# Optimization experiments

Measured on AMD Instinct MI355X. Metric: run time of the kernel, lower is better.

## Reference

```python
import jax, jax.numpy as jnp
import numpy as np

M, N, D, P = 16, 4096, 128, 8192
H = N // D


def setup_inputs() -> dict:
    key = jax.random.key(0)
    ks = jax.random.split(key, 6)
    return {
        "X": jax.random.normal(ks[0], (M, N), dtype=jnp.float32),
        "W_q": jax.random.normal(ks[1], (N, N), dtype=jnp.float32) / np.sqrt(N),
        "W_k": jax.random.normal(ks[2], (N, N), dtype=jnp.float32) / np.sqrt(N),
        "W_v": jax.random.normal(ks[3], (N, N), dtype=jnp.float32) / np.sqrt(N),
        "cache_K": jax.random.normal(ks[4], (H, P, D), dtype=jnp.float32),
        "cache_V": jax.random.normal(ks[5], (H, P, D), dtype=jnp.float32),
    }


def _rms(x):
    # unaffine RMS norm over last dim, no eps (matches torch source)
    return x * jax.lax.rsqrt(jnp.mean(jnp.square(x), axis=-1, keepdims=True))


def reference(X, W_q, W_k, W_v, cache_K, cache_V):
    m, n = X.shape
    h, p, d = cache_K.shape
    # QKV projections -> [H, M, D]
    q = (X @ W_q).reshape(m, h, d).swapaxes(0, 1)
    k = (X @ W_k).reshape(m, h, d).swapaxes(0, 1)
    v = (X @ W_v).reshape(m, h, d).swapaxes(0, 1)
    q_norm = _rms(q)
    k_norm = _rms(k)
    # prepend KV cache: [H, P+M, D]
    k_cache = jnp.concatenate([cache_K[:, :p, :], k_norm], axis=1)
    v_cache = jnp.concatenate([cache_V[:, :p, :], v], axis=1)
    # attention WITHOUT 1/sqrt(D) scaling (matches torch source)
    scores = jnp.einsum("hmd,hpd->hmp", q_norm, k_cache)
    weights = jax.nn.softmax(scores, axis=-1)
    out = jnp.einsum("hmp,hpd->hmd", weights, v_cache)  # [H, M, D]
    return out.swapaxes(0, 1).reshape(m, n)
```

## Files before the change

### kernel.cpp

```cpp
#include <hip/hip_runtime.h>
#include <hip/hip_bf16.h>
#include <math.h>

#define M_ 16
#define N_ 4096
#define D_ 128
#define P_ 8192
#define H_ 32

#define NIC 32
#define ICH (N_/NIC)
#define NCB 16

#define CHUNK 64
#define NCH (P_/CHUNK)
#define NCH1 (NCH+1)

#define QKV_SZ       (3*H_*M_*D_)
#define PART_OFF     (QKV_SZ)
#define OPART_OFF    (QKV_SZ)
#define OPART_HALFSZ ((H_*NCH1*M_*D_)/2)
#define ML_OFF       (OPART_OFF + OPART_HALFSZ)

__global__ __launch_bounds__(256) void k_proj(const float* __restrict__ X,
                                              const float* __restrict__ Wq,
                                              const float* __restrict__ Wk,
                                              const float* __restrict__ Wv,
                                              float* __restrict__ part) {
  const int mat = blockIdx.z;
  const float* __restrict__ W = (mat == 0) ? Wq : ((mat == 1) ? Wk : Wv);
  const int cb = blockIdx.x, ic = blockIdx.y;
  const int t = threadIdx.x;
  const int j0 = cb * 256 + t;
  const int i0 = ic * ICH;

  __shared__ __align__(16) float XT[ICH][20];

  {
    const int i_l = t & 127, mh = t >> 7;
#pragma unroll
    for (int r = 0; r < 8; ++r)
      XT[i_l][mh * 8 + r] = X[(size_t)(mh * 8 + r) * N_ + i0 + i_l];
  }
  __syncthreads();

  float acc[16];
#pragma unroll
  for (int m = 0; m < 16; ++m) acc[m] = 0.f;

#pragma unroll 8
  for (int i = 0; i < ICH; ++i) {
    const float wv = __builtin_nontemporal_load(W + (size_t)(i0 + i) * N_ + j0);
    float xr[16];
    {
      float4 xv;
      xv = *reinterpret_cast<const float4*>(&XT[i][0]);
      xr[0] = xv.x; xr[1] = xv.y; xr[2] = xv.z; xr[3] = xv.w;
      xv = *reinterpret_cast<const float4*>(&XT[i][4]);
      xr[4] = xv.x; xr[5] = xv.y; xr[6] = xv.z; xr[7] = xv.w;
      xv = *reinterpret_cast<const float4*>(&XT[i][8]);
      xr[8] = xv.x; xr[9] = xv.y; xr[10] = xv.z; xr[11] = xv.w;
      xv = *reinterpret_cast<const float4*>(&XT[i][12]);
      xr[12] = xv.x; xr[13] = xv.y; xr[14] = xv.z; xr[15] = xv.w;
    }
#pragma unroll
    for (int m = 0; m < 16; ++m) acc[m] = fmaf(xr[m], wv, acc[m]);
  }

#pragma unroll
  for (int m = 0; m < 16; ++m)
    __builtin_nontemporal_store(acc[m], part + (size_t)((mat * NIC + ic) * M_ + m) * N_ + j0);
}

__global__ __launch_bounds__(256) void k_reduce(const float* __restrict__ part,
                                                float* __restrict__ qkv) {
  const int mat = blockIdx.z, m = blockIdx.y, nc = blockIdx.x;
  const int t = threadIdx.x;
  const int n = nc * 256 + t;

  float s = 0.f;
#pragma unroll
  for (int ic = 0; ic < NIC; ++ic)
    s += __builtin_nontemporal_load(part + (size_t)((mat * NIC + ic) * M_ + m) * N_ + n);

  float ss = s * s;
#pragma unroll
  for (int off = 1; off < 64; off <<= 1) ss += __shfl_xor(ss, off);
  __shared__ float wsum[4];
  const int wave = t >> 6, lane = t & 63;
  if (lane == 0) wsum[wave] = ss;
  __syncthreads();
  const int half = t >> 7;
  const float tot = wsum[half * 2] + wsum[half * 2 + 1];
  const float scale = (mat < 2) ? rsqrtf(tot * (1.0f / 128.0f)) : 1.0f;

  const int h = n >> 7, d = n & 127;
  qkv[(size_t)((mat * H_ + h) * M_ + m) * D_ + d] = s * scale;
}

__device__ __forceinline__ float fold8(float a[8], int dq) {
#pragma unroll
  for (int i = 0; i < 4; ++i) {
    const float send = (dq & 4) ? a[i] : a[i + 4];
    const float recv = __shfl_xor(send, 4);
    a[i] = ((dq & 4) ? a[i + 4] : a[i]) + recv;
  }
#pragma unroll
  for (int i = 0; i < 2; ++i) {
    const float send = (dq & 2) ? a[i] : a[i + 2];
    const float recv = __shfl_xor(send, 2);
    a[i] = ((dq & 2) ? a[i + 2] : a[i]) + recv;
  }
  {
    const float send = (dq & 1) ? a[0] : a[1];
    const float recv = __shfl_xor(send, 1);
    a[0] = ((dq & 1) ? a[1] : a[0]) + recv;
  }
  return a[0];
}

__device__ __forceinline__ unsigned pk2(float a, float b) {
  __hip_bfloat16 ha = __float2bfloat16(a), hb = __float2bfloat16(b);
  const unsigned short ua = *reinterpret_cast<unsigned short*>(&ha);
  const unsigned short ub = *reinterpret_cast<unsigned short*>(&hb);
  return (unsigned)ua | ((unsigned)ub << 16);
}

__global__ __attribute__((amdgpu_waves_per_eu(2, 8)))
__launch_bounds__(256) void k_attn(const float* __restrict__ cacheK,
                                   const float* __restrict__ cacheV,
                                   const float* __restrict__ qkv,
                                   __hip_bfloat16* __restrict__ opart,
                                   float* __restrict__ ml) {
  const int c = blockIdx.x, h = blockIdx.y;
  const int t = threadIdx.x;
  const int wave = t >> 6, lane = t & 63;
  const int valid = (c < NCH) ? CHUNK : M_;
  const float* __restrict__ Ksrc = (c < NCH)
      ? (cacheK + ((size_t)h * P_ + (size_t)c * CHUNK) * D_)
      : (qkv + (size_t)((1 * H_ + h) * M_) * D_);
  const float* __restrict__ Vsrc = (c < NCH)
      ? (cacheV + ((size_t)h * P_ + (size_t)c * CHUNK) * D_)
      : (qkv + (size_t)((2 * H_ + h) * M_) * D_);

  __shared__ __align__(16) float smem[4096];
  __shared__ __align__(16) float wx[4 * 128];
  __shared__ __align__(16) float mlx[4][8][2];

  float* qs = smem;
  float* wxp = wx + wave * 128;

  {
    const float4* src = reinterpret_cast<const float4*>(qkv + (size_t)(h * M_) * D_);
    reinterpret_cast<float4*>(qs)[t] = src[t];
    reinterpret_cast<float4*>(qs)[t + 256] = src[t + 256];
  }
  __syncthreads();

  const int pg = lane >> 3, dq = lane & 7;
  const int dl = lane * 2;
  const int rg = wave >> 1, mbase = (wave & 1) * 8;
  const int rbase = rg * 32;
  int rc = valid - rbase; rc = (rc < 0) ? 0 : ((rc > 32) ? 32 : rc);
  const int nb = rc >> 3;

  float mrun = -3.0e38f, lrun = 0.f;
  float2 o[8];
#pragma unroll
  for (int mi = 0; mi < 8; ++mi) o[mi] = make_float2(0.f, 0.f);

#pragma unroll 1
  for (int b = 0; b < nb; ++b) {
    const int r0 = rbase + b * 8;

    float4 kk0, kk1, kk2, kk3;
    {
      const float* ka = Ksrc + (size_t)(r0 + pg) * D_ + dq * 4;
      kk0 = *reinterpret_cast<const float4*>(ka);
      kk1 = *reinterpret_cast<const float4*>(ka + 32);
      kk2 = *reinterpret_cast<const float4*>(ka + 64);
      kk3 = *reinterpret_cast<const float4*>(ka + 96);
    }
    float2 vv[8];
#pragma unroll
    for (int j = 0; j < 8; ++j)
      vv[j] = *reinterpret_cast<const float2*>(Vsrc + (size_t)(r0 + j) * D_ + dl);

    float a[8];
#pragma unroll
    for (int mi = 0; mi < 8; ++mi) {
      const float* qrow = qs + (mbase + mi) * D_ + dq * 4;
      const float4 q0 = *reinterpret_cast<const float4*>(qrow);
      const float4 q1 = *reinterpret_cast<const float4*>(qrow + 32);
      const float4 q2 = *reinterpret_cast<const float4*>(qrow + 64);
      const float4 q3 = *reinterpret_cast<const float4*>(qrow + 96);
      float s;
      s = q0.x * kk0.x;
      s = fmaf(q0.y, kk0.y, s); s = fmaf(q0.z, kk0.z, s); s = fmaf(q0.w, kk0.w, s);
      s = fmaf(q1.x, kk1.x, s); s = fmaf(q1.y, kk1.y, s);
      s = fmaf(q1.z, kk1.z, s); s = fmaf(q1.w, kk1.w, s);
      s = fmaf(q2.x, kk2.x, s); s = fmaf(q2.y, kk2.y, s);
      s = fmaf(q2.z, kk2.z, s); s = fmaf(q2.w, kk2.w, s);
      s = fmaf(q3.x, kk3.x, s); s = fmaf(q3.y, kk3.y, s);
      s = fmaf(q3.z, kk3.z, s); s = fmaf(q3.w, kk3.w, s);
      a[mi] = s;
    }

    const float sA = fold8(a, dq);
    float tmax = sA;
    tmax = fmaxf(tmax, __shfl_xor(tmax, 8));
    tmax = fmaxf(tmax, __shfl_xor(tmax, 16));
    tmax = fmaxf(tmax, __shfl_xor(tmax, 32));
    const float mnew = fmaxf(mrun, tmax);
    const float fc = __expf(mrun - mnew);
    mrun = mnew;
    const float wA = __expf(sA - mnew);
    float rs = wA;
    rs += __shfl_xor(rs, 8); rs += __shfl_xor(rs, 16); rs += __shfl_xor(rs, 32);
    lrun = lrun * fc + rs;

    wxp[pg * 8 + dq] = wA;

#pragma unroll
    for (int mi = 0; mi < 8; ++mi) {
      const float fcm = __shfl(fc, (lane & 56) | mi);
      o[mi].x *= fcm; o[mi].y *= fcm;
    }

#pragma unroll
    for (int j = 0; j < 8; ++j) {
      const float4 w0 = *reinterpret_cast<const float4*>(&wxp[j * 8]);
      const float4 w1 = *reinterpret_cast<const float4*>(&wxp[j * 8 + 4]);
      const float2 v = vv[j];
#define PVM(i, wc) o[i].x = fmaf(wc, v.x, o[i].x); o[i].y = fmaf(wc, v.y, o[i].y);
      PVM(0, w0.x) PVM(1, w0.y) PVM(2, w0.z) PVM(3, w0.w)
      PVM(4, w1.x) PVM(5, w1.y) PVM(6, w1.z) PVM(7, w1.w)
#undef PVM
    }
  }

  __syncthreads();
  float* obuf = smem;
#pragma unroll
  for (int mi = 0; mi < 8; ++mi)
    *reinterpret_cast<float2*>(&obuf[wave * 1024 + mi * 128 + dl]) = o[mi];
  if (lane < 8) { mlx[wave][lane][0] = mrun; mlx[wave][lane][1] = lrun; }
  __syncthreads();

  {
    const int mm = t >> 4, seg = t & 15;
    const int mh = mm >> 3, mi = mm & 7;
    const float m0v = mlx[mh][mi][0], m1v = mlx[2 + mh][mi][0];
    const float mstar = fmaxf(m0v, m1v);
    const float e0 = __expf(m0v - mstar), e1 = __expf(m1v - mstar);
    const float T = mlx[mh][mi][1] * e0 + mlx[2 + mh][mi][1] * e1;
    const float4 a0 = *reinterpret_cast<const float4*>(&obuf[mh * 1024 + mi * 128 + seg * 8]);
    const float4 a1 = *reinterpret_cast<const float4*>(&obuf[mh * 1024 + mi * 128 + seg * 8 + 4]);
    const float4 b0 = *reinterpret_cast<const float4*>(&obuf[(2 + mh) * 1024 + mi * 128 + seg * 8]);
    const float4 b1 = *reinterpret_cast<const float4*>(&obuf[(2 + mh) * 1024 + mi * 128 + seg * 8 + 4]);
    float r0 = e0 * a0.x + e1 * b0.x, r1 = e0 * a0.y + e1 * b0.y;
    float r2 = e0 * a0.z + e1 * b0.z, r3 = e0 * a0.w + e1 * b0.w;
    float r4 = e0 * a1.x + e1 * b1.x, r5 = e0 * a1.y + e1 * b1.y;
    float r6 = e0 * a1.z + e1 * b1.z, r7 = e0 * a1.w + e1 * b1.w;
    uint4 pk;
    pk.x = pk2(r0, r1); pk.y = pk2(r2, r3); pk.z = pk2(r4, r5); pk.w = pk2(r6, r7);
    const size_t base = ((size_t)(h * NCH1 + c) * M_ + mm) * D_ + seg * 8;
    *reinterpret_cast<uint4*>(opart + base) = pk;
    if (seg == 0) {
      ml[((size_t)(h * NCH1 + c) * M_ + mm) * 2 + 0] = mstar;
      ml[((size_t)(h * NCH1 + c) * M_ + mm) * 2 + 1] = T;
    }
  }
}

__global__ __launch_bounds__(128) void k_comb(const __hip_bfloat16* __restrict__ opart,
                                              const float* __restrict__ ml,
                                              float* __restrict__ out) {
  const int m = blockIdx.x, h = blockIdx.y, t = threadIdx.x;
  __shared__ float Ms[NCH1], Ls[NCH1];
  for (int i = t; i < NCH1; i += 128) {
    Ms[i] = ml[((size_t)(h * NCH1 + i) * M_ + m) * 2 + 0];
    Ls[i] = ml[((size_t)(h * NCH1 + i) * M_ + m) * 2 + 1];
  }
  __syncthreads();
  float gM = -3.0e38f;
#pragma unroll 8
  for (int c2 = 0; c2 < NCH1; ++c2) gM = fmaxf(gM, Ms[c2]);

  const __hip_bfloat16* __restrict__ ob =
      opart + (size_t)h * NCH1 * M_ * D_ + (size_t)m * D_ + t;
  float T = 0.f, o0 = 0.f, o1 = 0.f, o2 = 0.f, o3 = 0.f;
#pragma unroll 4
  for (int c2 = 0; c2 < NCH1 - 1; c2 += 4) {
    const float f0 = __expf(Ms[c2 + 0] - gM);
    const float f1 = __expf(Ms[c2 + 1] - gM);
    const float f2 = __expf(Ms[c2 + 2] - gM);
    const float f3 = __expf(Ms[c2 + 3] - gM);
    T = fmaf(Ls[c2 + 0], f0, T); T = fmaf(Ls[c2 + 1], f1, T);
    T = fmaf(Ls[c2 + 2], f2, T); T = fmaf(Ls[c2 + 3], f3, T);
    o0 = fmaf(__bfloat162float(ob[(size_t)(c2 + 0) * M_ * D_]), f0, o0);
    o1 = fmaf(__bfloat162float(ob[(size_t)(c2 + 1) * M_ * D_]), f1, o1);
    o2 = fmaf(__bfloat162float(ob[(size_t)(c2 + 2) * M_ * D_]), f2, o2);
    o3 = fmaf(__bfloat162float(ob[(size_t)(c2 + 3) * M_ * D_]), f3, o3);
  }
  {
    const int c2 = NCH1 - 1;
    const float f = __expf(Ms[c2] - gM);
    T = fmaf(Ls[c2], f, T);
    o0 = fmaf(__bfloat162float(ob[(size_t)c2 * M_ * D_]), f, o0);
  }
  out[(size_t)m * N_ + h * D_ + t] = (o0 + o1 + o2 + o3) / T;
}

extern "C" void kernel_launch(void* const* d_in, const int* in_sizes, int n_in,
                              void* d_out, int out_size, void* d_ws, size_t ws_size,
                              hipStream_t stream) {
  const float* X  = (const float*)d_in[0];
  const float* Wq = (const float*)d_in[1];
  const float* Wk = (const float*)d_in[2];
  const float* Wv = (const float*)d_in[3];
  const float* cK = (const float*)d_in[4];
  const float* cV = (const float*)d_in[5];
  float* ws    = (float*)d_ws;
  float* qkv   = ws;
  float* part  = ws + PART_OFF;
  __hip_bfloat16* opart = (__hip_bfloat16*)(ws + OPART_OFF);
  float* mlbuf = ws + ML_OFF;
  float* out   = (float*)d_out;

  hipLaunchKernelGGL(k_proj,   dim3(NCB, NIC, 3), dim3(256), 0, stream, X, Wq, Wk, Wv, part);
  hipLaunchKernelGGL(k_reduce, dim3(16, M_, 3),   dim3(256), 0, stream, part, qkv);
  hipLaunchKernelGGL(k_attn,   dim3(NCH1, H_),    dim3(256), 0, stream, cK, cV, qkv, opart, mlbuf);
  hipLaunchKernelGGL(k_comb,   dim3(M_, H_),      dim3(128), 0, stream, opart, mlbuf, out);
}
```

Before: 138.4 us.

## Overlap K/V projection with cache attention in one interleaved kernel

```diff
diff --git a/kernel.cpp b/kernel.cpp
--- a/kernel.cpp
+++ b/kernel.cpp
@@ -12,30 +12,32 @@
 #define ICH (N_/NIC)
 #define NCB 16
 
+#define NIC_KV 8
+#define ICH_KV (N_/NIC_KV)
+
 #define CHUNK 64
 #define NCH (P_/CHUNK)
 #define NCH1 (NCH+1)
 
 #define QKV_SZ       (3*H_*M_*D_)
-#define PART_OFF     (QKV_SZ)
 #define OPART_OFF    (QKV_SZ)
 #define OPART_HALFSZ ((H_*NCH1*M_*D_)/2)
+#define PART_Q_OFF   (OPART_OFF)
 #define ML_OFF       (OPART_OFF + OPART_HALFSZ)
+#define ML_SZ        (H_*NCH1*M_*2)
+#define PART_KV_OFF  (ML_OFF + ML_SZ)
+
+#define MAIN_BLOCKS 4352
 
 __global__ __launch_bounds__(256) void k_proj(const float* __restrict__ X,
                                               const float* __restrict__ Wq,
-                                              const float* __restrict__ Wk,
-                                              const float* __restrict__ Wv,
                                               float* __restrict__ part) {
-  const int mat = blockIdx.z;
-  const float* __restrict__ W = (mat == 0) ? Wq : ((mat == 1) ? Wk : Wv);
   const int cb = blockIdx.x, ic = blockIdx.y;
   const int t = threadIdx.x;
   const int j0 = cb * 256 + t;
   const int i0 = ic * ICH;
 
   __shared__ __align__(16) float XT[ICH][20];
-
   {
     const int i_l = t & 127, mh = t >> 7;
 #pragma unroll
@@ -50,7 +52,7 @@
 
 #pragma unroll 8
   for (int i = 0; i < ICH; ++i) {
-    const float wv = __builtin_nontemporal_load(W + (size_t)(i0 + i) * N_ + j0);
+    const float wv = __builtin_nontemporal_load(Wq + (size_t)(i0 + i) * N_ + j0);
     float xr[16];
     {
       float4 xv;
@@ -69,19 +71,20 @@
 
 #pragma unroll
   for (int m = 0; m < 16; ++m)
-    __builtin_nontemporal_store(acc[m], part + (size_t)((mat * NIC + ic) * M_ + m) * N_ + j0);
-}
-
-__global__ __launch_bounds__(256) void k_reduce(const float* __restrict__ part,
-                                                float* __restrict__ qkv) {
-  const int mat = blockIdx.z, m = blockIdx.y, nc = blockIdx.x;
+    __builtin_nontemporal_store(acc[m], part + (size_t)(ic * M_ + m) * N_ + j0);
+}
+
+__global__ __launch_bounds__(256) void k_reduce(const float* __restrict__ src,
+                                                float* __restrict__ qkv,
+                                                int nch, int mat_base) {
+  const int matL = blockIdx.z, m = blockIdx.y, nc = blockIdx.x;
+  const int mat = mat_base + matL;
   const int t = threadIdx.x;
   const int n = nc * 256 + t;
 
   float s = 0.f;
-#pragma unroll
-  for (int ic = 0; ic < NIC; ++ic)
-    s += __builtin_nontemporal_load(part + (size_t)((mat * NIC + ic) * M_ + m) * N_ + n);
+  for (int ic = 0; ic < nch; ++ic)
+    s += __builtin_nontemporal_load(src + (size_t)((matL * nch + ic) * M_ + m) * N_ + n);
 
   float ss = s * s;
 #pragma unroll
@@ -127,28 +130,78 @@
 }
 
 __global__ __attribute__((amdgpu_waves_per_eu(2, 8)))
-__launch_bounds__(256) void k_attn(const float* __restrict__ cacheK,
+__launch_bounds__(256) void k_main(const float* __restrict__ X,
+                                   const float* __restrict__ Wk,
+                                   const float* __restrict__ Wv,
+                                   const float* __restrict__ cacheK,
                                    const float* __restrict__ cacheV,
                                    const float* __restrict__ qkv,
+                                   float* __restrict__ part_kv,
                                    __hip_bfloat16* __restrict__ opart,
                                    float* __restrict__ ml) {
-  const int c = blockIdx.x, h = blockIdx.y;
+  __shared__ __align__(16) float shmem[4672];
+  const int bid = blockIdx.x;
   const int t = threadIdx.x;
+  const bool is_proj = (bid % 17) == 16;
+
+  if (is_proj) {
+    const int proj_id = bid / 17;
+    const int matL = proj_id >> 7;
+    const int ic = (proj_id >> 4) & 7;
+    const int cb = proj_id & 15;
+    const float* __restrict__ W = matL ? Wv : Wk;
+    const int j0 = cb * 256 + t;
+    float (*XT)[20] = reinterpret_cast<float (*)[20]>(shmem);
+
+    float acc[16];
+#pragma unroll
+    for (int m = 0; m < 16; ++m) acc[m] = 0.f;
+
+    for (int s4 = 0; s4 < 4; ++s4) {
+      const int i0 = ic * ICH_KV + s4 * 128;
+      __syncthreads();
+      {
+        const int i_l = t & 127, mh = t >> 7;
+#pragma unroll
+        for (int r = 0; r < 8; ++r)
+          XT[i_l][mh * 8 + r] = X[(size_t)(mh * 8 + r) * N_ + i0 + i_l];
+      }
+      __syncthreads();
+#pragma unroll 8
+      for (int i = 0; i < 128; ++i) {
+        const float wv = __builtin_nontemporal_load(W + (size_t)(i0 + i) * N_ + j0);
+        float xr[16];
+        {
+          float4 xv;
+          xv = *reinterpret_cast<const float4*>(&XT[i][0]);
+          xr[0] = xv.x; xr[1] = xv.y; xr[2] = xv.z; xr[3] = xv.w;
+          xv = *reinterpret_cast<const float4*>(&XT[i][4]);
+          xr[4] = xv.x; xr[5] = xv.y; xr[6] = xv.z; xr[7] = xv.w;
+          xv = *reinterpret_cast<const float4*>(&XT[i][8]);
+          xr[8] = xv.x; xr[9] = xv.y; xr[10] = xv.z; xr[11] = xv.w;
+          xv = *reinterpret_cast<const float4*>(&XT[i][12]);
+          xr[12] = xv.x; xr[13] = xv.y; xr[14] = xv.z; xr[15] = xv.w;
+        }
+#pragma unroll
+        for (int m = 0; m < 16; ++m) acc[m] = fmaf(xr[m], wv, acc[m]);
+      }
+    }
+#pragma unroll
+    for (int m = 0; m < 16; ++m)
+      __builtin_nontemporal_store(acc[m],
+          part_kv + (size_t)((matL * NIC_KV + ic) * M_ + m) * N_ + j0);
+    return;
+  }
+
+  const int attn_id = (bid / 17) * 16 + (bid % 17);
+  const int h = attn_id >> 7, c = attn_id & 127;
   const int wave = t >> 6, lane = t & 63;
-  const int valid = (c < NCH) ? CHUNK : M_;
-  const float* __restrict__ Ksrc = (c < NCH)
-      ? (cacheK + ((size_t)h * P_ + (size_t)c * CHUNK) * D_)
-      : (qkv + (size_t)((1 * H_ + h) * M_) * D_);
-  const float* __restrict__ Vsrc = (c < NCH)
-      ? (cacheV + ((size_t)h * P_ + (size_t)c * CHUNK) * D_)
-      : (qkv + (size_t)((2 * H_ + h) * M_) * D_);
-
-  __shared__ __align__(16) float smem[4096];
-  __shared__ __align__(16) float wx[4 * 128];
-  __shared__ __align__(16) float mlx[4][8][2];
-
-  float* qs = smem;
-  float* wxp = wx + wave * 128;
+  const float* __restrict__ Ksrc = cacheK + ((size_t)h * P_ + (size_t)c * CHUNK) * D_;
+  const float* __restrict__ Vsrc = cacheV + ((size_t)h * P_ + (size_t)c * CHUNK) * D_;
+
+  float* qs = shmem;
+  float* wxp = shmem + 4096 + wave * 128;
+  float* mlx = shmem + 4608;
 
   {
     const float4* src = reinterpret_cast<const float4*>(qkv + (size_t)(h * M_) * D_);
@@ -161,7 +214,150 @@
   const int dl = lane * 2;
   const int rg = wave >> 1, mbase = (wave & 1) * 8;
   const int rbase = rg * 32;
-  int rc = valid - rbase; rc = (rc < 0) ? 0 : ((rc > 32) ? 32 : rc);
+
+  float mrun = -3.0e38f, lrun = 0.f;
+  float2 o[8];
+#pragma unroll
+  for (int mi = 0; mi < 8; ++mi) o[mi] = make_float2(0.f, 0.f);
+
+  float4 kkA[4], kkB[4];
+  float2 vvA[8], vvB[8];
+
+  auto kload = [&](float4 (&kk)[4], int r0) {
+    const float* ka = Ksrc + (size_t)(r0 + pg) * D_ + dq * 4;
+    kk[0] = *reinterpret_cast<const float4*>(ka);
+    kk[1] = *reinterpret_cast<const float4*>(ka + 32);
+    kk[2] = *reinterpret_cast<const float4*>(ka + 64);
+    kk[3] = *reinterpret_cast<const float4*>(ka + 96);
+  };
+  auto vload = [&](float2 (&vv)[8], int r0) {
+#pragma unroll
+    for (int j = 0; j < 8; ++j)
+      vv[j] = *reinterpret_cast<const float2*>(Vsrc + (size_t)(r0 + j) * D_ + dl);
+  };
+  auto body = [&](float4 (&kk)[4], float2 (&vv)[8]) {
+    float a[8];
+#pragma unroll
+    for (int mi = 0; mi < 8; ++mi) {
+      const float* qrow = qs + (mbase + mi) * D_ + dq * 4;
+      const float4 q0 = *reinterpret_cast<const float4*>(qrow);
+      const float4 q1 = *reinterpret_cast<const float4*>(qrow + 32);
+      const float4 q2 = *reinterpret_cast<const float4*>(qrow + 64);
+      const float4 q3 = *reinterpret_cast<const float4*>(qrow + 96);
+      float s;
+      s = q0.x * kk[0].x;
+      s = fmaf(q0.y, kk[0].y, s); s = fmaf(q0.z, kk[0].z, s); s = fmaf(q0.w, kk[0].w, s);
+      s = fmaf(q1.x, kk[1].x, s); s = fmaf(q1.y, kk[1].y, s);
+      s = fmaf(q1.z, kk[1].z, s); s = fmaf(q1.w, kk[1].w, s);
+      s = fmaf(q2.x, kk[2].x, s); s = fmaf(q2.y, kk[2].y, s);
+      s = fmaf(q2.z, kk[2].z, s); s = fmaf(q2.w, kk[2].w, s);
+      s = fmaf(q3.x, kk[3].x, s); s = fmaf(q3.y, kk[3].y, s);
+      s = fmaf(q3.z, kk[3].z, s); s = fmaf(q3.w, kk[3].w, s);
+      a[mi] = s;
+    }
+    const float sA = fold8(a, dq);
+    float tmax = sA;
+    tmax = fmaxf(tmax, __shfl_xor(tmax, 8));
+    tmax = fmaxf(tmax, __shfl_xor(tmax, 16));
+    tmax = fmaxf(tmax, __shfl_xor(tmax, 32));
+    const float mnew = fmaxf(mrun, tmax);
+    const float fc = __expf(mrun - mnew);
+    mrun = mnew;
+    const float wA = __expf(sA - mnew);
+    float rs = wA;
+    rs += __shfl_xor(rs, 8); rs += __shfl_xor(rs, 16); rs += __shfl_xor(rs, 32);
+    lrun = lrun * fc + rs;
+    wxp[pg * 8 + dq] = wA;
+#pragma unroll
+    for (int mi = 0; mi < 8; ++mi) {
+      const float fcm = __shfl(fc, (lane & 56) | mi);
+      o[mi].x *= fcm; o[mi].y *= fcm;
+    }
+#pragma unroll
+    for (int j = 0; j < 8; ++j) {
+      const float4 w0 = *reinterpret_cast<const float4*>(&wxp[j * 8]);
+      const float4 w1 = *reinterpret_cast<const float4*>(&wxp[j * 8 + 4]);
+      const float2 v = vv[j];
+#define PVM(i, wc) o[i].x = fmaf(wc, v.x, o[i].x); o[i].y = fmaf(wc, v.y, o[i].y);
+      PVM(0, w0.x) PVM(1, w0.y) PVM(2, w0.z) PVM(3, w0.w)
+      PVM(4, w1.x) PVM(5, w1.y) PVM(6, w1.z) PVM(7, w1.w)
+#undef PVM
+    }
+  };
+
+  kload(kkA, rbase);      vload(vvA, rbase);
+  kload(kkB, rbase + 8);  vload(vvB, rbase + 8);
+  body(kkA, vvA);
+  kload(kkA, rbase + 16); vload(vvA, rbase + 16);
+  body(kkB, vvB);
+  kload(kkB, rbase + 24); vload(vvB, rbase + 24);
+  body(kkA, vvA);
+  body(kkB, vvB);
+
+  __syncthreads();
+  float* obuf = shmem;
+#pragma unroll
+  for (int mi = 0; mi < 8; ++mi)
+    *reinterpret_cast<float2*>(&obuf[wave * 1024 + mi * 128 + dl]) = o[mi];
+  if (lane < 8) { mlx[(wave * 8 + lane) * 2] = mrun; mlx[(wave * 8 + lane) * 2 + 1] = lrun; }
+  __syncthreads();
+
+  {
+    const int mm = t >> 4, seg = t & 15;
+    const int mh = mm >> 3, mi = mm & 7;
+    const float m0v = mlx[(mh * 8 + mi) * 2], m1v = mlx[((2 + mh) * 8 + mi) * 2];
+    const float mstar = fmaxf(m0v, m1v);
+    const float e0 = __expf(m0v - mstar), e1 = __expf(m1v - mstar);
+    const float T = mlx[(mh * 8 + mi) * 2 + 1] * e0 + mlx[((2 + mh) * 8 + mi) * 2 + 1] * e1;
+    const float4 a0 = *reinterpret_cast<const float4*>(&obuf[mh * 1024 + mi * 128 + seg * 8]);
+    const float4 a1 = *reinterpret_cast<const float4*>(&obuf[mh * 1024 + mi * 128 + seg * 8 + 4]);
+    const float4 b0 = *reinterpret_cast<const float4*>(&obuf[(2 + mh) * 1024 + mi * 128 + seg * 8]);
+    const float4 b1 = *reinterpret_cast<const float4*>(&obuf[(2 + mh) * 1024 + mi * 128 + seg * 8 + 4]);
+    float r0 = e0 * a0.x + e1 * b0.x, r1 = e0 * a0.y + e1 * b0.y;
+    float r2 = e0 * a0.z + e1 * b0.z, r3 = e0 * a0.w + e1 * b0.w;
+    float r4 = e0 * a1.x + e1 * b1.x, r5 = e0 * a1.y + e1 * b1.y;
+    float r6 = e0 * a1.z + e1 * b1.z, r7 = e0 * a1.w + e1 * b1.w;
+    uint4 pk;
+    pk.x = pk2(r0, r1); pk.y = pk2(r2, r3); pk.z = pk2(r4, r5); pk.w = pk2(r6, r7);
+    const size_t base = ((size_t)(h * NCH1 + c) * M_ + mm) * D_ + seg * 8;
+    *reinterpret_cast<uint4*>(opart + base) = pk;
+    if (seg == 0) {
+      ml[((size_t)(h * NCH1 + c) * M_ + mm) * 2 + 0] = mstar;
+      ml[((size_t)(h * NCH1 + c) * M_ + mm) * 2 + 1] = T;
+    }
+  }
+}
+
+__global__ __attribute__((amdgpu_waves_per_eu(2, 8)))
+__launch_bounds__(256) void k_attn_tail(const float* __restrict__ qkv,
+                                        __hip_bfloat16* __restrict__ opart,
+                                        float* __restrict__ ml) {
+  const int h = blockIdx.y;
+  const int c = NCH;
+  const int t = threadIdx.x;
+  const int wave = t >> 6, lane = t & 63;
+  const int valid = M_;
+  const float* __restrict__ Ksrc = qkv + (size_t)((1 * H_ + h) * M_) * D_;
+  const float* __restrict__ Vsrc = qkv + (size_t)((2 * H_ + h) * M_) * D_;
+
+  __shared__ __align__(16) float smem[4096];
+  __shared__ __align__(16) float wx[4 * 128];
+  __shared__ __align__(16) float mlx[4][8][2];
+  float* qs = smem;
+  float* wxp = wx + wave * 128;
+
+  {
+    const float4* src = reinterpret_cast<const float4*>(qkv + (size_t)(h * M_) * D_);
+    reinterpret_cast<float4*>(qs)[t] = src[t];
+    reinterpret_cast<float4*>(qs)[t + 256] = src[t + 256];
+  }
+  __syncthreads();
+
+  const int pg = lane >> 3, dq = lane & 7;
+  const int dl = lane * 2;
+  const int rg = wave >> 1, mbase = (wave & 1) * 8;
+  const int rbase = rg * 32;
+  int rc = valid - rbase; rc = (rc < 0) ? 0 : rc;
   const int nb = rc >> 3;
 
   float mrun = -3.0e38f, lrun = 0.f;
@@ -172,7 +368,6 @@
 #pragma unroll 1
   for (int b = 0; b < nb; ++b) {
     const int r0 = rbase + b * 8;
-
     float4 kk0, kk1, kk2, kk3;
     {
       const float* ka = Ksrc + (size_t)(r0 + pg) * D_ + dq * 4;
@@ -205,7 +400,6 @@
       s = fmaf(q3.z, kk3.z, s); s = fmaf(q3.w, kk3.w, s);
       a[mi] = s;
     }
-
     const float sA = fold8(a, dq);
     float tmax = sA;
     tmax = fmaxf(tmax, __shfl_xor(tmax, 8));
@@ -218,15 +412,12 @@
     float rs = wA;
     rs += __shfl_xor(rs, 8); rs += __shfl_xor(rs, 16); rs += __shfl_xor(rs, 32);
     lrun = lrun * fc + rs;
-
     wxp[pg * 8 + dq] = wA;
-
 #pragma unroll
     for (int mi = 0; mi < 8; ++mi) {
       const float fcm = __shfl(fc, (lane & 56) | mi);
       o[mi].x *= fcm; o[mi].y *= fcm;
     }
-
 #pragma unroll
     for (int j = 0; j < 8; ++j) {
       const float4 w0 = *reinterpret_cast<const float4*>(&wxp[j * 8]);
@@ -321,15 +512,19 @@
   const float* Wv = (const float*)d_in[3];
   const float* cK = (const float*)d_in[4];
   const float* cV = (const float*)d_in[5];
-  float* ws    = (float*)d_ws;
-  float* qkv   = ws;
-  float* part  = ws + PART_OFF;
+  float* ws     = (float*)d_ws;
+  float* qkv    = ws;
+  float* part_q = ws + PART_Q_OFF;
   __hip_bfloat16* opart = (__hip_bfloat16*)(ws + OPART_OFF);
-  float* mlbuf = ws + ML_OFF;
-  float* out   = (float*)d_out;
-
-  hipLaunchKernelGGL(k_proj,   dim3(NCB, NIC, 3), dim3(256), 0, stream, X, Wq, Wk, Wv, part);
-  hipLaunchKernelGGL(k_reduce, dim3(16, M_, 3),   dim3(256), 0, stream, part, qkv);
-  hipLaunchKernelGGL(k_attn,   dim3(NCH1, H_),    dim3(256), 0, stream, cK, cV, qkv, opart, mlbuf);
-  hipLaunchKernelGGL(k_comb,   dim3(M_, H_),      dim3(128), 0, stream, opart, mlbuf, out);
-}
+  float* mlbuf  = ws + ML_OFF;
+  float* part_kv = ws + PART_KV_OFF;
+  float* out    = (float*)d_out;
+
+  hipLaunchKernelGGL(k_proj,      dim3(NCB, NIC, 1), dim3(256), 0, stream, X, Wq, part_q);
+  hipLaunchKernelGGL(k_reduce,    dim3(16, M_, 1),   dim3(256), 0, stream, part_q, qkv, NIC, 0);
+  hipLaunchKernelGGL(k_main,      dim3(MAIN_BLOCKS), dim3(256), 0, stream,
+                     X, Wk, Wv, cK, cV, qkv, part_kv, opart, mlbuf);
+  hipLaunchKernelGGL(k_reduce,    dim3(16, M_, 2),   dim3(256), 0, stream, part_kv, qkv, NIC_KV, 1);
+  hipLaunchKernelGGL(k_attn_tail, dim3(1, H_),       dim3(256), 0, stream, qkv, opart, mlbuf);
+  hipLaunchKernelGGL(k_comb,      dim3(M_, H_),      dim3(128), 0, stream, opart, mlbuf, out);
+}
```

After: 288.1 us. +108.2%, slower.
